# Optimization experiments

Measured on AMD Instinct MI355X. Metric: run time of the kernel, lower is better.

The kernel has to match this reference:

```python
import jax, jax.numpy as jnp
import numpy as np

B, N, D_IN, D_OUT = 4, 2048, 1024, 1024

def setup_inputs() -> dict:
    key = jax.random.key(0)
    ks = jax.random.split(key, 7)
    s_in = 1.0 / np.sqrt(D_IN)
    return {
        "X": jax.random.normal(ks[0], (B, N, D_IN), dtype=jnp.float32),
        "Wq": jax.random.uniform(ks[1], (D_IN, D_OUT), jnp.float32, -s_in, s_in),
        "bq": jax.random.uniform(ks[2], (D_OUT,), jnp.float32, -s_in, s_in),
        "Wk": jax.random.uniform(ks[3], (D_IN, D_OUT), jnp.float32, -s_in, s_in),
        "bk": jax.random.uniform(ks[4], (D_OUT,), jnp.float32, -s_in, s_in),
        "Wv": jax.random.uniform(ks[5], (D_IN, D_OUT), jnp.float32, -s_in, s_in),
        "bv": jax.random.uniform(ks[6], (D_OUT,), jnp.float32, -s_in, s_in),
    }

def reference(X, Wq, bq, Wk, bk, Wv, bv):
    # QKV projections: [B,N,D_in] @ [D_in,D_out] -> [B,N,D_out]
    q = jnp.einsum('bnd,de->bne', X, Wq) + bq
    k = jnp.einsum('bnd,de->bne', X, Wk) + bk
    v = jnp.einsum('bnd,de->bne', X, Wv) + bv
    # Unscaled attention (faithful: original has no 1/sqrt(d))
    scores = jnp.einsum('bne,bme->bnm', q, k)  # [B,N,N]
    weights = jax.nn.softmax(scores, axis=-1)
    return jnp.einsum('bnm,bme->bne', weights, v)
```

## Files before the change

kernel.cpp:

```cpp
#include <hip/hip_runtime.h>
#include <hip/hip_bf16.h>
#include <hip/hip_fp16.h>
#include <stdint.h>


typedef unsigned short ushort_t;
typedef __attribute__((ext_vector_type(8))) _Float16  f16x8;
typedef __attribute__((ext_vector_type(4))) _Float16  f16x4;
typedef __attribute__((ext_vector_type(4))) float     f32x4;

__device__ __forceinline__ void store_out(float* p, float v) { *p = v; }
__device__ __forceinline__ void store_out(__half* p, float v) { *p = __float2half(v); }

__device__ __forceinline__ void async_load16(const void* g, void* l) {
  __builtin_amdgcn_global_load_lds(
      (const __attribute__((address_space(1))) void*)g,
      (__attribute__((address_space(3))) void*)l, 16, 0, 0);
}

template <typename OutT>
__global__ __launch_bounds__(256)
void gemm_bt_kernel(const ushort_t* __restrict__ A, const ushort_t* __restrict__ BT,
                    OutT* __restrict__ C, int N, int K,
                    long batchA, long batchB, long batchC)
{
  __shared__ ushort_t As[2][128 * 32];
  __shared__ ushort_t Bs[2][128 * 32];

  const int t    = threadIdx.x;
  const int lane = t & 63;
  const int wave = t >> 6;
  const int wm   = (wave >> 1) * 64;
  const int wn   = (wave & 1) * 64;

  const ushort_t* Ab = A + (long)blockIdx.z * batchA + (long)blockIdx.y * 128 * K;
  const ushort_t* Bb = BT + (long)blockIdx.z * batchB + (long)blockIdx.x * 128 * K;
  OutT* Cb = C + (long)blockIdx.z * batchC;

  const int ldr = t >> 2;
  const int swzs = (ldr & 3) ^ ((ldr >> 2) & 3);
  const int ldc = ((t & 3) ^ swzs) * 8;
  const int frow = lane & 15;
  const int fsz  = (frow & 3) ^ ((frow >> 2) & 3);
  const int fo   = (((lane >> 4) ^ fsz)) * 8;

  f32x4 acc[4][4];
  const f32x4 zero = {0.0f, 0.0f, 0.0f, 0.0f};
#pragma unroll
  for (int i = 0; i < 4; ++i)
#pragma unroll
    for (int j = 0; j < 4; ++j) acc[i][j] = zero;

  for (int k0 = 0; k0 < K; k0 += 64) {
    __syncthreads();
    const ushort_t* ga = Ab + (long)ldr * K + k0 + ldc;
    const ushort_t* gb = Bb + (long)ldr * K + k0 + ldc;
#pragma unroll
    for (int h = 0; h < 2; ++h) {
      async_load16(ga + h * 32,                &As[h][t * 8]);
      async_load16(ga + h * 32 + 64 * (long)K, &As[h][2048 + t * 8]);
      async_load16(gb + h * 32,                &Bs[h][t * 8]);
      async_load16(gb + h * 32 + 64 * (long)K, &Bs[h][2048 + t * 8]);
    }
    __syncthreads();
#pragma unroll
    for (int h = 0; h < 2; ++h) {
      f16x8 af[4], bf[4];
#pragma unroll
      for (int i = 0; i < 4; ++i) {
        af[i] = *(const f16x8*)&As[h][(wm + i * 16 + frow) * 32 + fo];
        bf[i] = *(const f16x8*)&Bs[h][(wn + i * 16 + frow) * 32 + fo];
      }
#pragma unroll
      for (int mi = 0; mi < 4; ++mi)
#pragma unroll
        for (int ni = 0; ni < 4; ++ni)
          acc[mi][ni] = __builtin_amdgcn_mfma_f32_16x16x32_f16(af[mi], bf[ni], acc[mi][ni], 0, 0, 0);
    }
  }

  const int er = (lane >> 4) * 4;
  const int ec = lane & 15;
#pragma unroll
  for (int ni = 0; ni < 4; ++ni) {
    const int gcol = blockIdx.x * 128 + wn + ni * 16 + ec;
#pragma unroll
    for (int mi = 0; mi < 4; ++mi) {
#pragma unroll
      for (int r = 0; r < 4; ++r) {
        const long grow = (long)blockIdx.y * 128 + wm + mi * 16 + er + r;
        store_out(&Cb[grow * (long)N + gcol], acc[mi][ni][r]);
      }
    }
  }
}

__global__ __launch_bounds__(256)
void qkv_gemm_kernel(const ushort_t* __restrict__ A, const ushort_t* __restrict__ BT,
                     const float* __restrict__ bq, const float* __restrict__ bk,
                     const float* __restrict__ bvp,
                     __half* __restrict__ Qh, __half* __restrict__ Kh,
                     ushort_t* __restrict__ Vt)
{
  const int K = 1024;
  __shared__ ushort_t As[2][128 * 32];
  __shared__ ushort_t Bs[2][128 * 32];

  const int t    = threadIdx.x;
  const int lane = t & 63;
  const int wave = t >> 6;
  const int wm   = (wave >> 1) * 64;
  const int wn   = (wave & 1) * 64;

  const ushort_t* Ab = A + (long)blockIdx.y * 128 * K;
  const ushort_t* Bb = BT + (long)blockIdx.x * 128 * K;

  const int ldr = t >> 2;
  const int swzs = (ldr & 3) ^ ((ldr >> 2) & 3);
  const int ldc = ((t & 3) ^ swzs) * 8;
  const int frow = lane & 15;
  const int fsz  = (frow & 3) ^ ((frow >> 2) & 3);
  const int fo   = (((lane >> 4) ^ fsz)) * 8;

  f32x4 acc[4][4];
  const f32x4 zero = {0.0f, 0.0f, 0.0f, 0.0f};
#pragma unroll
  for (int i = 0; i < 4; ++i)
#pragma unroll
    for (int j = 0; j < 4; ++j) acc[i][j] = zero;

  for (int k0 = 0; k0 < K; k0 += 64) {
    __syncthreads();
    const ushort_t* ga = Ab + (long)ldr * K + k0 + ldc;
    const ushort_t* gb = Bb + (long)ldr * K + k0 + ldc;
#pragma unroll
    for (int h = 0; h < 2; ++h) {
      async_load16(ga + h * 32,                &As[h][t * 8]);
      async_load16(ga + h * 32 + 64 * (long)K, &As[h][2048 + t * 8]);
      async_load16(gb + h * 32,                &Bs[h][t * 8]);
      async_load16(gb + h * 32 + 64 * (long)K, &Bs[h][2048 + t * 8]);
    }
    __syncthreads();
#pragma unroll
    for (int h = 0; h < 2; ++h) {
      f16x8 af[4], bf[4];
#pragma unroll
      for (int i = 0; i < 4; ++i) {
        af[i] = *(const f16x8*)&As[h][(wm + i * 16 + frow) * 32 + fo];
        bf[i] = *(const f16x8*)&Bs[h][(wn + i * 16 + frow) * 32 + fo];
      }
#pragma unroll
      for (int mi = 0; mi < 4; ++mi)
#pragma unroll
        for (int ni = 0; ni < 4; ++ni)
          acc[mi][ni] = __builtin_amdgcn_mfma_f32_16x16x32_f16(af[mi], bf[ni], acc[mi][ni], 0, 0, 0);
    }
  }

  const int er = (lane >> 4) * 4;
  const int ec = lane & 15;
  const int tgt = blockIdx.x >> 3;
  const float* bias = (tgt == 0) ? bq : (tgt == 1) ? bk : bvp;
#pragma unroll
  for (int ni = 0; ni < 4; ++ni) {
    const int c = (blockIdx.x & 7) * 128 + wn + ni * 16 + ec;
    const float bval = bias[c];
#pragma unroll
    for (int mi = 0; mi < 4; ++mi) {
      const long grow0 = (long)blockIdx.y * 128 + wm + mi * 16 + er;
      if (tgt < 2) {
        __half* o = (tgt == 0) ? Qh : Kh;
#pragma unroll
        for (int r = 0; r < 4; ++r)
          o[(grow0 + r) * 1024 + c] = __float2half(acc[mi][ni][r] + bval);
      } else {
        const long b  = grow0 >> 11;
        const long ml = grow0 & 2047;
        f16x4 v4;
#pragma unroll
        for (int r = 0; r < 4; ++r) v4[r] = (_Float16)(acc[mi][ni][r] + bval);
        *(f16x4*)&Vt[b * 2097152 + (long)c * 2048 + ml] = v4;
      }
    }
  }
}

__global__ __launch_bounds__(256)
void cvt_f32_f16_kernel(const float* __restrict__ src, __half* __restrict__ dst, long n)
{
  const long i = ((long)blockIdx.x * 256 + threadIdx.x) * 8;
  if (i + 8 > n) return;
  const float4 a = *(const float4*)(src + i);
  const float4 b = *(const float4*)(src + i + 4);
  f16x8 h;
  h[0] = (_Float16)a.x; h[1] = (_Float16)a.y; h[2] = (_Float16)a.z; h[3] = (_Float16)a.w;
  h[4] = (_Float16)b.x; h[5] = (_Float16)b.y; h[6] = (_Float16)b.z; h[7] = (_Float16)b.w;
  *(f16x8*)((ushort_t*)dst + i) = h;
}

__global__ __launch_bounds__(256)
void transpose_cvt3_kernel(const float* __restrict__ W0, const float* __restrict__ W1,
                           const float* __restrict__ W2, __half* __restrict__ dst)
{
  __shared__ float tile[32][33];
  const int z = blockIdx.z;
  const float* src = (z == 0) ? W0 : (z == 1) ? W1 : W2;
  __half* d = dst + (long)z * 1024 * 1024;
  const int c0 = blockIdx.x * 32;
  const int r0 = blockIdx.y * 32;
  const int tx = threadIdx.x & 31;
  const int ty = threadIdx.x >> 5;
#pragma unroll
  for (int i = 0; i < 32; i += 8)
    tile[ty + i][tx] = src[(long)(r0 + ty + i) * 1024 + (c0 + tx)];
  __syncthreads();
#pragma unroll
  for (int i = 0; i < 32; i += 8)
    d[(long)(c0 + ty + i) * 1024 + (r0 + tx)] = __float2half(tile[tx][ty + i]);
}

__global__ __launch_bounds__(256)
void softmax2048_kernel(const float* __restrict__ S, __half* __restrict__ P)
{
  const long row = blockIdx.x;
  const float* s = S + row * 2048;
  const int t = threadIdx.x;

  const float4 a = ((const float4*)s)[t * 2];
  const float4 b = ((const float4*)s)[t * 2 + 1];
  float v[8] = {a.x, a.y, a.z, a.w, b.x, b.y, b.z, b.w};

  float mx = v[0];
#pragma unroll
  for (int i = 1; i < 8; ++i) mx = fmaxf(mx, v[i]);
#pragma unroll
  for (int off = 32; off > 0; off >>= 1) mx = fmaxf(mx, __shfl_xor(mx, off, 64));

  __shared__ float redm[4], reds[4];
  if ((t & 63) == 0) redm[t >> 6] = mx;
  __syncthreads();
  mx = fmaxf(fmaxf(redm[0], redm[1]), fmaxf(redm[2], redm[3]));

  float sum = 0.0f;
#pragma unroll
  for (int i = 0; i < 8; ++i) { v[i] = __expf(v[i] - mx); sum += v[i]; }
#pragma unroll
  for (int off = 32; off > 0; off >>= 1) sum += __shfl_xor(sum, off, 64);
  if ((t & 63) == 0) reds[t >> 6] = sum;
  __syncthreads();
  sum = reds[0] + reds[1] + reds[2] + reds[3];

  const float inv = 1.0f / sum;
  f16x8 h;
#pragma unroll
  for (int i = 0; i < 8; ++i) h[i] = (_Float16)(v[i] * inv);
  *(f16x8*)((ushort_t*)P + row * 2048 + t * 8) = h;
}

extern "C" void kernel_launch(void* const* d_in, const int* in_sizes, int n_in,
                              void* d_out, int out_size, void* d_ws, size_t ws_size,
                              hipStream_t stream)
{
  const int  Bb = 4, Nn = 2048, Dd = 1024;
  const long BN = (long)Bb * Nn;

  const float* X  = (const float*)d_in[0];
  const float* Wq = (const float*)d_in[1];
  const float* bq = (const float*)d_in[2];
  const float* Wk = (const float*)d_in[3];
  const float* bk = (const float*)d_in[4];
  const float* Wv = (const float*)d_in[5];
  const float* bv = (const float*)d_in[6];
  float* Out      = (float*)d_out;

  uint8_t* w = (uint8_t*)d_ws;
  ushort_t* Wt = (ushort_t*)w;  w += (size_t)3 * Dd * Dd * 2;

  transpose_cvt3_kernel<<<dim3(Dd / 32, Dd / 32, 3), 256, 0, stream>>>(Wq, Wk, Wv, (__half*)Wt);

  const size_t fullNeed = (size_t)3 * Dd * Dd * 2
                        + 4 * ((size_t)BN * Dd * 2)
                        + (size_t)Bb * Nn * Nn * 4
                        + (size_t)Bb * Nn * Nn * 2;

  if (ws_size >= fullNeed) {
    ushort_t* Xh = (ushort_t*)w;  w += (size_t)BN * Dd * 2;
    ushort_t* Q  = (ushort_t*)w;  w += (size_t)BN * Dd * 2;
    ushort_t* Kb = (ushort_t*)w;  w += (size_t)BN * Dd * 2;
    ushort_t* Vt = (ushort_t*)w;  w += (size_t)BN * Dd * 2;
    float*    S  = (float*)w;     w += (size_t)Bb * Nn * Nn * 4;
    ushort_t* P  = (ushort_t*)w;

    cvt_f32_f16_kernel<<<dim3((unsigned)(BN * Dd / (8 * 256))), 256, 0, stream>>>(
        X, (__half*)Xh, BN * Dd);

    qkv_gemm_kernel<<<dim3(3 * Dd / 128, BN / 128, 1), 256, 0, stream>>>(
        Xh, Wt, bq, bk, bv, (__half*)Q, (__half*)Kb, Vt);

    gemm_bt_kernel<float><<<dim3(Nn / 128, Nn / 128, Bb), 256, 0, stream>>>(
        Q, Kb, S, Nn, Dd, (long)Nn * Dd, (long)Nn * Dd, (long)Nn * Nn);

    softmax2048_kernel<<<dim3((unsigned)(Bb * (long)Nn)), 256, 0, stream>>>(S, (__half*)P);

    gemm_bt_kernel<float><<<dim3(Dd / 128, Nn / 128, Bb), 256, 0, stream>>>(
        P, Vt, Out, Dd, Nn, (long)Nn * Nn, (long)Dd * Nn, (long)Nn * Dd);
  } else {
    ushort_t* Xh = (ushort_t*)w;  w += (size_t)Nn * Dd * 2;
    ushort_t* Q  = (ushort_t*)w;  w += (size_t)Nn * Dd * 2;
    ushort_t* Kb = (ushort_t*)w;  w += (size_t)Nn * Dd * 2;
    ushort_t* Vt = (ushort_t*)w;  w += (size_t)Nn * Dd * 2;
    float*    S  = (float*)w;     w += (size_t)Nn * Nn * 4;
    ushort_t* P  = (ushort_t*)w;

    for (int b = 0; b < Bb; ++b) {
      const float* Xb = X + (long)b * Nn * Dd;
      cvt_f32_f16_kernel<<<dim3((unsigned)((long)Nn * Dd / (8 * 256))), 256, 0, stream>>>(
          Xb, (__half*)Xh, (long)Nn * Dd);
      qkv_gemm_kernel<<<dim3(3 * Dd / 128, Nn / 128, 1), 256, 0, stream>>>(
          Xh, Wt, bq, bk, bv, (__half*)Q, (__half*)Kb, Vt);
      gemm_bt_kernel<float><<<dim3(Nn / 128, Nn / 128, 1), 256, 0, stream>>>(
          Q, Kb, S, Nn, Dd, 0, 0, 0);
      softmax2048_kernel<<<dim3(Nn), 256, 0, stream>>>(S, (__half*)P);
      gemm_bt_kernel<float><<<dim3(Dd / 128, Nn / 128, 1), 256, 0, stream>>>(
          P, Vt, Out + (long)b * Nn * Dd, Dd, Nn, 0, 0, 0);
    }
  }
}
```

Baseline: 302.7 us.

## Fuse softmax into QK GEMM epilogue with per-tile stats and rescale in PV

The QK^T GEMM epilogue now computes per-64-column-chunk row maxima and exp-sums and writes locally exponentiated scores as fp16 instead of fp32 logits. A small reduce kernel merges the chunk stats into per-chunk scale factors, and the PV GEMM applies those scales to the A fragments while loading. This removes the separate softmax pass and halves the size of the score matrix. Each chunk is exponentiated against its local max, so values stay in fp16 range, but an extra fp16 multiply per fragment in the PV inner loop adds rounding and ALU work.

```diff
diff --git a/kernel.cpp b/kernel.cpp
--- a/kernel.cpp
+++ b/kernel.cpp
@@ -2,6 +2,7 @@
 #include <hip/hip_bf16.h>
 #include <hip/hip_fp16.h>
 #include <stdint.h>
+#include <math.h>
 
 
 typedef unsigned short ushort_t;
@@ -9,21 +10,20 @@
 typedef __attribute__((ext_vector_type(4))) _Float16  f16x4;
 typedef __attribute__((ext_vector_type(4))) float     f32x4;
 
-__device__ __forceinline__ void store_out(float* p, float v) { *p = v; }
-__device__ __forceinline__ void store_out(__half* p, float v) { *p = __float2half(v); }
-
 __device__ __forceinline__ void async_load16(const void* g, void* l) {
   __builtin_amdgcn_global_load_lds(
       (const __attribute__((address_space(1))) void*)g,
       (__attribute__((address_space(3))) void*)l, 16, 0, 0);
 }
 
-template <typename OutT>
-__global__ __launch_bounds__(256)
-void gemm_bt_kernel(const ushort_t* __restrict__ A, const ushort_t* __restrict__ BT,
-                    OutT* __restrict__ C, int N, int K,
-                    long batchA, long batchB, long batchC)
-{
+__global__ __launch_bounds__(256)
+void qkv_gemm_kernel(const ushort_t* __restrict__ A, const ushort_t* __restrict__ BT,
+                     const float* __restrict__ bq, const float* __restrict__ bk,
+                     const float* __restrict__ bvp,
+                     __half* __restrict__ Qh, __half* __restrict__ Kh,
+                     ushort_t* __restrict__ Vt)
+{
+  const int K = 1024;
   __shared__ ushort_t As[2][128 * 32];
   __shared__ ushort_t Bs[2][128 * 32];
 
@@ -33,9 +33,8 @@
   const int wm   = (wave >> 1) * 64;
   const int wn   = (wave & 1) * 64;
 
-  const ushort_t* Ab = A + (long)blockIdx.z * batchA + (long)blockIdx.y * 128 * K;
-  const ushort_t* Bb = BT + (long)blockIdx.z * batchB + (long)blockIdx.x * 128 * K;
-  OutT* Cb = C + (long)blockIdx.z * batchC;
+  const ushort_t* Ab = A + (long)blockIdx.y * 128 * K;
+  const ushort_t* Bb = BT + (long)blockIdx.x * 128 * K;
 
   const int ldr = t >> 2;
   const int swzs = (ldr & 3) ^ ((ldr >> 2) & 3);
@@ -81,26 +80,35 @@
 
   const int er = (lane >> 4) * 4;
   const int ec = lane & 15;
+  const int tgt = blockIdx.x >> 3;
+  const float* bias = (tgt == 0) ? bq : (tgt == 1) ? bk : bvp;
 #pragma unroll
   for (int ni = 0; ni < 4; ++ni) {
-    const int gcol = blockIdx.x * 128 + wn + ni * 16 + ec;
+    const int c = (blockIdx.x & 7) * 128 + wn + ni * 16 + ec;
+    const float bval = bias[c];
 #pragma unroll
     for (int mi = 0; mi < 4; ++mi) {
-#pragma unroll
-      for (int r = 0; r < 4; ++r) {
-        const long grow = (long)blockIdx.y * 128 + wm + mi * 16 + er + r;
-        store_out(&Cb[grow * (long)N + gcol], acc[mi][ni][r]);
-      }
-    }
-  }
-}
-
-__global__ __launch_bounds__(256)
-void qkv_gemm_kernel(const ushort_t* __restrict__ A, const ushort_t* __restrict__ BT,
-                     const float* __restrict__ bq, const float* __restrict__ bk,
-                     const float* __restrict__ bvp,
-                     __half* __restrict__ Qh, __half* __restrict__ Kh,
-                     ushort_t* __restrict__ Vt)
+      const long grow0 = (long)blockIdx.y * 128 + wm + mi * 16 + er;
+      if (tgt < 2) {
+        __half* o = (tgt == 0) ? Qh : Kh;
+#pragma unroll
+        for (int r = 0; r < 4; ++r)
+          o[(grow0 + r) * 1024 + c] = __float2half(acc[mi][ni][r] + bval);
+      } else {
+        const long b  = grow0 >> 11;
+        const long ml = grow0 & 2047;
+        f16x4 v4;
+#pragma unroll
+        for (int r = 0; r < 4; ++r) v4[r] = (_Float16)(acc[mi][ni][r] + bval);
+        *(f16x4*)&Vt[b * 2097152 + (long)c * 2048 + ml] = v4;
+      }
+    }
+  }
+}
+
+__global__ __launch_bounds__(256)
+void qk_gemm_kernel(const ushort_t* __restrict__ Q, const ushort_t* __restrict__ Kh,
+                    __half* __restrict__ S, float* __restrict__ PM, float* __restrict__ PS)
 {
   const int K = 1024;
   __shared__ ushort_t As[2][128 * 32];
@@ -111,9 +119,11 @@
   const int wave = t >> 6;
   const int wm   = (wave >> 1) * 64;
   const int wn   = (wave & 1) * 64;
-
-  const ushort_t* Ab = A + (long)blockIdx.y * 128 * K;
-  const ushort_t* Bb = BT + (long)blockIdx.x * 128 * K;
+  const long z   = blockIdx.z;
+
+  const ushort_t* Ab = Q + z * 2048 * 1024 + (long)blockIdx.y * 128 * K;
+  const ushort_t* Bb = Kh + z * 2048 * 1024 + (long)blockIdx.x * 128 * K;
+  __half* Sb = S + z * 2048 * 2048;
 
   const int ldr = t >> 2;
   const int swzs = (ldr & 3) ^ ((ldr >> 2) & 3);
@@ -159,27 +169,150 @@
 
   const int er = (lane >> 4) * 4;
   const int ec = lane & 15;
-  const int tgt = blockIdx.x >> 3;
-  const float* bias = (tgt == 0) ? bq : (tgt == 1) ? bk : bvp;
+  const int cc = blockIdx.x * 2 + (wave & 1);
+  float* PMb = PM + z * 32 * 2048 + (long)cc * 2048;
+  float* PSb = PS + z * 32 * 2048 + (long)cc * 2048;
+
+#pragma unroll
+  for (int mi = 0; mi < 4; ++mi)
+#pragma unroll
+    for (int r = 0; r < 4; ++r) {
+      float m = fmaxf(fmaxf(acc[mi][0][r], acc[mi][1][r]),
+                      fmaxf(acc[mi][2][r], acc[mi][3][r]));
+      m = fmaxf(m, __shfl_xor(m, 1));
+      m = fmaxf(m, __shfl_xor(m, 2));
+      m = fmaxf(m, __shfl_xor(m, 4));
+      m = fmaxf(m, __shfl_xor(m, 8));
+      float s = 0.0f;
+#pragma unroll
+      for (int ni = 0; ni < 4; ++ni) {
+        const float e = __expf(acc[mi][ni][r] - m);
+        acc[mi][ni][r] = e;
+        s += e;
+      }
+      s += __shfl_xor(s, 1);
+      s += __shfl_xor(s, 2);
+      s += __shfl_xor(s, 4);
+      s += __shfl_xor(s, 8);
+      if (ec == 0) {
+        const long row = (long)blockIdx.y * 128 + wm + mi * 16 + er + r;
+        PMb[row] = m;
+        PSb[row] = s;
+      }
+    }
+
 #pragma unroll
   for (int ni = 0; ni < 4; ++ni) {
-    const int c = (blockIdx.x & 7) * 128 + wn + ni * 16 + ec;
-    const float bval = bias[c];
+    const long col = (long)blockIdx.x * 128 + wn + ni * 16 + ec;
+#pragma unroll
+    for (int mi = 0; mi < 4; ++mi)
+#pragma unroll
+      for (int r = 0; r < 4; ++r) {
+        const long grow = (long)blockIdx.y * 128 + wm + mi * 16 + er + r;
+        Sb[grow * 2048 + col] = __float2half(acc[mi][ni][r]);
+      }
+  }
+}
+
+__global__ __launch_bounds__(256)
+void softmax_reduce_kernel(const float* __restrict__ PM, const float* __restrict__ PS,
+                           float* __restrict__ Sc)
+{
+  const int r = blockIdx.x * 256 + threadIdx.x;
+  const int b = r >> 11, row = r & 2047;
+  const long base = (long)b * 32 * 2048 + row;
+  float m = -3.4e38f;
+#pragma unroll
+  for (int cb = 0; cb < 32; ++cb) m = fmaxf(m, PM[base + cb * 2048]);
+  float l = 0.0f;
+#pragma unroll
+  for (int cb = 0; cb < 32; ++cb) l += PS[base + cb * 2048] * __expf(PM[base + cb * 2048] - m);
+  const float inv = 1.0f / l;
+#pragma unroll
+  for (int cb = 0; cb < 32; ++cb) Sc[base + cb * 2048] = __expf(PM[base + cb * 2048] - m) * inv;
+}
+
+__global__ __launch_bounds__(256)
+void pv_gemm_kernel(const ushort_t* __restrict__ S, const ushort_t* __restrict__ Vt,
+                    const float* __restrict__ Sc, float* __restrict__ Out)
+{
+  const int K = 2048;
+  __shared__ ushort_t As[2][128 * 32];
+  __shared__ ushort_t Bs[2][128 * 32];
+
+  const int t    = threadIdx.x;
+  const int lane = t & 63;
+  const int wave = t >> 6;
+  const int wm   = (wave >> 1) * 64;
+  const int wn   = (wave & 1) * 64;
+  const long z   = blockIdx.z;
+
+  const ushort_t* Ab = S + z * 2048 * 2048 + (long)blockIdx.y * 128 * K;
+  const ushort_t* Bb = Vt + z * 1024 * 2048 + (long)blockIdx.x * 128 * K;
+  const float* Scb = Sc + z * 32 * 2048;
+  float* Cb = Out + z * 2048 * 1024;
+
+  const int ldr = t >> 2;
+  const int swzs = (ldr & 3) ^ ((ldr >> 2) & 3);
+  const int ldc = ((t & 3) ^ swzs) * 8;
+  const int frow = lane & 15;
+  const int fsz  = (frow & 3) ^ ((frow >> 2) & 3);
+  const int fo   = (((lane >> 4) ^ fsz)) * 8;
+
+  const int arow0 = blockIdx.y * 128 + wm + frow;
+
+  f32x4 acc[4][4];
+  const f32x4 zero = {0.0f, 0.0f, 0.0f, 0.0f};
+#pragma unroll
+  for (int i = 0; i < 4; ++i)
+#pragma unroll
+    for (int j = 0; j < 4; ++j) acc[i][j] = zero;
+
+  for (int k0 = 0; k0 < K; k0 += 64) {
+    const int cb = k0 >> 6;
+    _Float16 sc16[4];
+#pragma unroll
+    for (int i = 0; i < 4; ++i)
+      sc16[i] = (_Float16)Scb[(long)cb * 2048 + arow0 + i * 16];
+
+    __syncthreads();
+    const ushort_t* ga = Ab + (long)ldr * K + k0 + ldc;
+    const ushort_t* gb = Bb + (long)ldr * K + k0 + ldc;
+#pragma unroll
+    for (int h = 0; h < 2; ++h) {
+      async_load16(ga + h * 32,                &As[h][t * 8]);
+      async_load16(ga + h * 32 + 64 * (long)K, &As[h][2048 + t * 8]);
+      async_load16(gb + h * 32,                &Bs[h][t * 8]);
+      async_load16(gb + h * 32 + 64 * (long)K, &Bs[h][2048 + t * 8]);
+    }
+    __syncthreads();
+#pragma unroll
+    for (int h = 0; h < 2; ++h) {
+      f16x8 af[4], bf[4];
+#pragma unroll
+      for (int i = 0; i < 4; ++i) {
+        af[i] = *(const f16x8*)&As[h][(wm + i * 16 + frow) * 32 + fo] * sc16[i];
+        bf[i] = *(const f16x8*)&Bs[h][(wn + i * 16 + frow) * 32 + fo];
+      }
+#pragma unroll
+      for (int mi = 0; mi < 4; ++mi)
+#pragma unroll
+        for (int ni = 0; ni < 4; ++ni)
+          acc[mi][ni] = __builtin_amdgcn_mfma_f32_16x16x32_f16(af[mi], bf[ni], acc[mi][ni], 0, 0, 0);
+    }
+  }
+
+  const int er = (lane >> 4) * 4;
+  const int ec = lane & 15;
+#pragma unroll
+  for (int ni = 0; ni < 4; ++ni) {
+    const int gcol = blockIdx.x * 128 + wn + ni * 16 + ec;
 #pragma unroll
     for (int mi = 0; mi < 4; ++mi) {
-      const long grow0 = (long)blockIdx.y * 128 + wm + mi * 16 + er;
-      if (tgt < 2) {
-        __half* o = (tgt == 0) ? Qh : Kh;
-#pragma unroll
-        for (int r = 0; r < 4; ++r)
-          o[(grow0 + r) * 1024 + c] = __float2half(acc[mi][ni][r] + bval);
-      } else {
-        const long b  = grow0 >> 11;
-        const long ml = grow0 & 2047;
-        f16x4 v4;
-#pragma unroll
-        for (int r = 0; r < 4; ++r) v4[r] = (_Float16)(acc[mi][ni][r] + bval);
-        *(f16x4*)&Vt[b * 2097152 + (long)c * 2048 + ml] = v4;
+#pragma unroll
+      for (int r = 0; r < 4; ++r) {
+        const long grow = (long)blockIdx.y * 128 + wm + mi * 16 + er + r;
+        Cb[grow * 1024 + gcol] = acc[mi][ni][r];
       }
     }
   }
@@ -219,44 +352,6 @@
     d[(long)(c0 + ty + i) * 1024 + (r0 + tx)] = __float2half(tile[tx][ty + i]);
 }
 
-__global__ __launch_bounds__(256)
-void softmax2048_kernel(const float* __restrict__ S, __half* __restrict__ P)
-{
-  const long row = blockIdx.x;
-  const float* s = S + row * 2048;
-  const int t = threadIdx.x;
-
-  const float4 a = ((const float4*)s)[t * 2];
-  const float4 b = ((const float4*)s)[t * 2 + 1];
-  float v[8] = {a.x, a.y, a.z, a.w, b.x, b.y, b.z, b.w};
-
-  float mx = v[0];
-#pragma unroll
-  for (int i = 1; i < 8; ++i) mx = fmaxf(mx, v[i]);
-#pragma unroll
-  for (int off = 32; off > 0; off >>= 1) mx = fmaxf(mx, __shfl_xor(mx, off, 64));
-
-  __shared__ float redm[4], reds[4];
-  if ((t & 63) == 0) redm[t >> 6] = mx;
-  __syncthreads();
-  mx = fmaxf(fmaxf(redm[0], redm[1]), fmaxf(redm[2], redm[3]));
-
-  float sum = 0.0f;
-#pragma unroll
-  for (int i = 0; i < 8; ++i) { v[i] = __expf(v[i] - mx); sum += v[i]; }
-#pragma unroll
-  for (int off = 32; off > 0; off >>= 1) sum += __shfl_xor(sum, off, 64);
-  if ((t & 63) == 0) reds[t >> 6] = sum;
-  __syncthreads();
-  sum = reds[0] + reds[1] + reds[2] + reds[3];
-
-  const float inv = 1.0f / sum;
-  f16x8 h;
-#pragma unroll
-  for (int i = 0; i < 8; ++i) h[i] = (_Float16)(v[i] * inv);
-  *(f16x8*)((ushort_t*)P + row * 2048 + t * 8) = h;
-}
-
 extern "C" void kernel_launch(void* const* d_in, const int* in_sizes, int n_in,
                               void* d_out, int out_size, void* d_ws, size_t ws_size,
                               hipStream_t stream)
@@ -278,18 +373,21 @@
 
   transpose_cvt3_kernel<<<dim3(Dd / 32, Dd / 32, 3), 256, 0, stream>>>(Wq, Wk, Wv, (__half*)Wt);
 
+  const size_t statsBytes = (size_t)Bb * 32 * Nn * 4;
   const size_t fullNeed = (size_t)3 * Dd * Dd * 2
                         + 4 * ((size_t)BN * Dd * 2)
-                        + (size_t)Bb * Nn * Nn * 4
-                        + (size_t)Bb * Nn * Nn * 2;
+                        + (size_t)Bb * Nn * Nn * 2
+                        + 3 * statsBytes;
 
   if (ws_size >= fullNeed) {
     ushort_t* Xh = (ushort_t*)w;  w += (size_t)BN * Dd * 2;
     ushort_t* Q  = (ushort_t*)w;  w += (size_t)BN * Dd * 2;
     ushort_t* Kb = (ushort_t*)w;  w += (size_t)BN * Dd * 2;
     ushort_t* Vt = (ushort_t*)w;  w += (size_t)BN * Dd * 2;
-    float*    S  = (float*)w;     w += (size_t)Bb * Nn * Nn * 4;
-    ushort_t* P  = (ushort_t*)w;
+    ushort_t* S  = (ushort_t*)w;  w += (size_t)Bb * Nn * Nn * 2;
+    float*    PM = (float*)w;     w += statsBytes;
+    float*    PS = (float*)w;     w += statsBytes;
+    float*    Sc = (float*)w;
 
     cvt_f32_f16_kernel<<<dim3((unsigned)(BN * Dd / (8 * 256))), 256, 0, stream>>>(
         X, (__half*)Xh, BN * Dd);
@@ -297,20 +395,22 @@
     qkv_gemm_kernel<<<dim3(3 * Dd / 128, BN / 128, 1), 256, 0, stream>>>(
         Xh, Wt, bq, bk, bv, (__half*)Q, (__half*)Kb, Vt);
 
-    gemm_bt_kernel<float><<<dim3(Nn / 128, Nn / 128, Bb), 256, 0, stream>>>(
-        Q, Kb, S, Nn, Dd, (long)Nn * Dd, (long)Nn * Dd, (long)Nn * Nn);
-
-    softmax2048_kernel<<<dim3((unsigned)(Bb * (long)Nn)), 256, 0, stream>>>(S, (__half*)P);
-
-    gemm_bt_kernel<float><<<dim3(Dd / 128, Nn / 128, Bb), 256, 0, stream>>>(
-        P, Vt, Out, Dd, Nn, (long)Nn * Nn, (long)Dd * Nn, (long)Nn * Dd);
+    qk_gemm_kernel<<<dim3(Nn / 128, Nn / 128, Bb), 256, 0, stream>>>(
+        Q, Kb, (__half*)S, PM, PS);
+
+    softmax_reduce_kernel<<<dim3((unsigned)(Bb * Nn / 256)), 256, 0, stream>>>(PM, PS, Sc);
+
+    pv_gemm_kernel<<<dim3(Dd / 128, Nn / 128, Bb), 256, 0, stream>>>(
+        S, Vt, Sc, Out);
   } else {
     ushort_t* Xh = (ushort_t*)w;  w += (size_t)Nn * Dd * 2;
     ushort_t* Q  = (ushort_t*)w;  w += (size_t)Nn * Dd * 2;
     ushort_t* Kb = (ushort_t*)w;  w += (size_t)Nn * Dd * 2;
     ushort_t* Vt = (ushort_t*)w;  w += (size_t)Nn * Dd * 2;
-    float*    S  = (float*)w;     w += (size_t)Nn * Nn * 4;
-    ushort_t* P  = (ushort_t*)w;
+    ushort_t* S  = (ushort_t*)w;  w += (size_t)Nn * Nn * 2;
+    float*    PM = (float*)w;     w += (size_t)32 * Nn * 4;
+    float*    PS = (float*)w;     w += (size_t)32 * Nn * 4;
+    float*    Sc = (float*)w;
 
     for (int b = 0; b < Bb; ++b) {
       const float* Xb = X + (long)b * Nn * Dd;
@@ -318,11 +418,11 @@
           Xb, (__half*)Xh, (long)Nn * Dd);
       qkv_gemm_kernel<<<dim3(3 * Dd / 128, Nn / 128, 1), 256, 0, stream>>>(
           Xh, Wt, bq, bk, bv, (__half*)Q, (__half*)Kb, Vt);
-      gemm_bt_kernel<float><<<dim3(Nn / 128, Nn / 128, 1), 256, 0, stream>>>(
-          Q, Kb, S, Nn, Dd, 0, 0, 0);
-      softmax2048_kernel<<<dim3(Nn), 256, 0, stream>>>(S, (__half*)P);
-      gemm_bt_kernel<float><<<dim3(Dd / 128, Nn / 128, 1), 256, 0, stream>>>(
-          P, Vt, Out + (long)b * Nn * Dd, Dd, Nn, 0, 0, 0);
-    }
-  }
-}
+      qk_gemm_kernel<<<dim3(Nn / 128, Nn / 128, 1), 256, 0, stream>>>(
+          Q, Kb, (__half*)S, PM, PS);
+      softmax_reduce_kernel<<<dim3((unsigned)(Nn / 256)), 256, 0, stream>>>(PM, PS, Sc);
+      pv_gemm_kernel<<<dim3(Dd / 128, Nn / 128, 1), 256, 0, stream>>>(
+          S, Vt, Sc, Out + (long)b * Nn * Dd);
+    }
+  }
+}
```

Result: faster. 273.6 us (-9.6%).
